# Kernel tuning notes

Hardware: AMD Instinct MI355X
Metric: run time of the kernel (lower is better)

## Reference

```python
import jax, jax.numpy as jnp
import numpy as np

N_MLPS = 256
N_BLOCKS = 8
TCODE = 13
IN_F = 3
HID = 128
OUT_F = 1
B = 256
NPTS = 2048
K = 256  # 8-bit codebook
OMEGA = 30.0

# per-layer (fan_in, fan_out) for weight reconstruction
LAYER_SHAPES = [(IN_F + TCODE, HID), (HID, HID), (HID, HID), (HID, OUT_F)]


def setup_inputs() -> dict:
    key = jax.random.key(0)
    ks = jax.random.split(key, 20)
    inp = {
        "x": jax.random.uniform(ks[0], (B, NPTS, IN_F), jnp.float32, -1.0, 1.0),
        "mlp_idx": jax.random.randint(ks[1], (B,), 0, N_MLPS, jnp.int32),
        "block_idx": jax.random.randint(ks[2], (B,), 0, N_BLOCKS, jnp.int32),
        "latent_table": jax.random.normal(ks[3], (N_MLPS, N_BLOCKS, TCODE), jnp.float32),
    }
    for l, (fi, fo) in enumerate(LAYER_SHAPES):
        bound = 1.0 / np.sqrt(fi)
        inp[f"centroids_l{l}"] = jax.random.uniform(ks[4 + 3 * l], (K,), jnp.float32, -bound, bound)
        inp[f"labels_l{l}"] = jax.random.randint(ks[5 + 3 * l], (N_MLPS * fi * fo,), 0, K, jnp.int32)
        inp[f"bias_l{l}"] = jax.random.uniform(ks[6 + 3 * l], (N_MLPS, 1, fo), jnp.float32, -bound, bound)
    return inp


def _layer(h, idx, centroids, labels, bias, fi, fo, apply_sin):
    # codebook dequant: weight.view(-1)[:] = centroids[labels]
    weight = centroids[labels].reshape(N_MLPS, fi, fo)
    # indexed bmm: torch.bmm(x, weight[indices]) + bias[indices]
    out = jnp.einsum("bni,bio->bno", h, weight[idx]) + bias[idx]
    return jnp.sin(OMEGA * out) if apply_sin else out


def reference(x, mlp_idx, block_idx, latent_table,
              centroids_l0, labels_l0, bias_l0,
              centroids_l1, labels_l1, bias_l1,
              centroids_l2, labels_l2, bias_l2,
              centroids_l3, labels_l3, bias_l3):
    # gather per-sample latent code and concat with coords
    z = latent_table[mlp_idx, block_idx]                      # [B, TCODE]
    h = jnp.concatenate(
        [x, jnp.broadcast_to(z[:, None, :], (x.shape[0], x.shape[1], TCODE))], axis=-1)
    cs = [centroids_l0, centroids_l1, centroids_l2, centroids_l3]
    ls = [labels_l0, labels_l1, labels_l2, labels_l3]
    bs = [bias_l0, bias_l1, bias_l2, bias_l3]
    for l, (fi, fo) in enumerate(LAYER_SHAPES):
        h = _layer(h, mlp_idx, cs[l], ls[l], bs[l], fi, fo, apply_sin=(l < len(LAYER_SHAPES) - 1))
    return h
```

## Files before the change

kernel.cpp:

```cpp
#include <hip/hip_runtime.h>


typedef unsigned int u32;
typedef unsigned short u16;
typedef __bf16 v8bf  __attribute__((ext_vector_type(8)));
typedef __bf16 v2bf  __attribute__((ext_vector_type(2)));
typedef float  v16f  __attribute__((ext_vector_type(16)));
typedef float  v2f   __attribute__((ext_vector_type(2)));
typedef u32    v4u   __attribute__((ext_vector_type(4)));
typedef u32    v2u   __attribute__((ext_vector_type(2)));

#define MFMA(a, b, c) __builtin_amdgcn_mfma_f32_32x32x16_bf16(a, b, c, 0, 0, 0)

#define HSTRIDE 128
#define OMEGA_S 4.774648292756860f

__device__ __forceinline__ float sinrev(float rev) {
    return __builtin_amdgcn_sinf(__builtin_amdgcn_fractf(rev));
}

__device__ __forceinline__ u32 pack2(float c) {
    __bf16 b0 = (__bf16)c;
    float  f0 = (float)b0;
    __bf16 b1 = (__bf16)(c - f0);
    return (u32)__builtin_bit_cast(u16, b0) |
           ((u32)__builtin_bit_cast(u16, b1) << 16);
}

__device__ __forceinline__ void pk2(float s0, float s1, u32& lo, u32& hi) {
    v2f s; s[0] = s0; s[1] = s1;
    v2bf l = __builtin_convertvector(s, v2bf);
    u32 lov = __builtin_bit_cast(u32, l);
    v2f lf;
    lf[0] = __builtin_bit_cast(float, lov << 16);
    lf[1] = __builtin_bit_cast(float, lov & 0xffff0000u);
    v2f r = s - lf;
    v2bf h = __builtin_convertvector(r, v2bf);
    lo = lov;
    hi = __builtin_bit_cast(u32, h);
}

__device__ __forceinline__ u32 pklo(float s0, float s1) {
    v2f s; s[0] = s0; s[1] = s1;
    v2bf l = __builtin_convertvector(s, v2bf);
    return __builtin_bit_cast(u32, l);
}

#define PLO(a, b) __builtin_amdgcn_perm((a), (b), 0x05040100u)
#define PHI(a, b) __builtin_amdgcn_perm((a), (b), 0x07060302u)

__global__ __launch_bounds__(512)
void ecnr_dequant(const float* __restrict__ cent0, const int* __restrict__ lab0,
                  const float* __restrict__ cent1, const int* __restrict__ lab1,
                  const float* __restrict__ cent2, const int* __restrict__ lab2,
                  const float* __restrict__ cent3, const int* __restrict__ lab3,
                  const float* __restrict__ bias0, const float* __restrict__ bias1,
                  const float* __restrict__ bias2,
                  u16* __restrict__ wpl1, u16* __restrict__ wpl2,
                  u16* __restrict__ w0pl, u16* __restrict__ w3pl,
                  float* __restrict__ biasc)
{
    __shared__ u32 cpk[512];
    const int t = threadIdx.x;

    if (blockIdx.x < 512) {
        const int m = blockIdx.x >> 1, L = blockIdx.x & 1;
        if (t < 256) cpk[t] = pack2((L ? cent2 : cent1)[t] * OMEGA_S);
        __syncthreads();
        const int* lab = (L ? lab2 : lab1) + (size_t)m * 16384;
        u16* base = (L ? wpl2 : wpl1) + (size_t)m * 32768;
        #pragma unroll
        for (int i = 0; i < 4; ++i) {
            const int id = i * 512 + t;
            const int n = id & 127, c = id >> 7;
            u32 g[8];
            #pragma unroll
            for (int j = 0; j < 8; ++j) g[j] = cpk[lab[(8 * c + j) * 128 + n]];
            v4u lo, hi;
            #pragma unroll
            for (int r = 0; r < 4; ++r) {
                lo[r] = PLO(g[2 * r + 1], g[2 * r]);
                hi[r] = PHI(g[2 * r + 1], g[2 * r]);
            }
            *(v4u*)(base + c * 1024 + n * 8)         = lo;
            *(v4u*)(base + 16384 + c * 1024 + n * 8) = hi;
        }
    } else {
        const int m = blockIdx.x - 512;
        if (t < 256) cpk[t] = pack2(cent0[t] * OMEGA_S);
        else         cpk[t] = pack2(cent3[t - 256]);
        __syncthreads();
        if (t < 256) {
            const int n = t & 127, c = t >> 7;
            const int* lab = lab0 + (size_t)m * 2048;
            u32 g[8];
            #pragma unroll
            for (int j = 0; j < 8; ++j) g[j] = cpk[lab[(8 * c + j) * 128 + n]];
            v4u lo, hi;
            #pragma unroll
            for (int r = 0; r < 4; ++r) {
                lo[r] = PLO(g[2 * r + 1], g[2 * r]);
                hi[r] = PHI(g[2 * r + 1], g[2 * r]);
            }
            u16* b0 = w0pl + (size_t)m * 4096;
            *(v4u*)(b0 + c * 1024 + n * 8)        = lo;
            *(v4u*)(b0 + 2048 + c * 1024 + n * 8) = hi;
        } else if (t < 384) {
            const int kk = t - 256;
            const u32 u = cpk[256 + lab3[(size_t)m * 128 + kk]];
            w3pl[(size_t)m * 256 + kk]       = (u16)u;
            w3pl[(size_t)m * 256 + 128 + kk] = (u16)(u >> 16);
        }
        if (t < 384) {
            const int li = t >> 7, kk = t & 127;
            const float* bsrc = (li == 0) ? bias0 : (li == 1) ? bias1 : bias2;
            biasc[(size_t)m * 384 + t] = bsrc[m * 128 + kk] * OMEGA_S;
        }
    }
}


#define EPI_FULL(ACC, ROWLO, ROWHI)                               \
    do {                                                          \
        _Pragma("unroll")                                         \
        for (int gg = 0; gg < 4; ++gg) {                          \
            const int wo = (((4 * nt + gg) ^ key) << 3) + 4 * q;  \
            const float s0 = sinrev((ACC)[4 * gg + 0]);           \
            const float s1 = sinrev((ACC)[4 * gg + 1]);           \
            const float s2 = sinrev((ACC)[4 * gg + 2]);           \
            const float s3 = sinrev((ACC)[4 * gg + 3]);           \
            u32 l0, h0, l1, h1;                                   \
            pk2(s0, s1, l0, h0);                                  \
            pk2(s2, s3, l1, h1);                                  \
            v2u lov, hiv;                                         \
            lov[0] = l0; lov[1] = l1;                             \
            hiv[0] = h0; hiv[1] = h1;                             \
            *(v2u*)((ROWLO) + wo) = lov;                          \
            *(v2u*)((ROWHI) + wo) = hiv;                          \
        }                                                         \
    } while (0)

#define EPI_LO(ACC, ROWLO)                                        \
    do {                                                          \
        _Pragma("unroll")                                         \
        for (int gg = 0; gg < 4; ++gg) {                          \
            const int wo = (((4 * nt + gg) ^ key) << 3) + 4 * q;  \
            const float s0 = sinrev((ACC)[4 * gg + 0]);           \
            const float s1 = sinrev((ACC)[4 * gg + 1]);           \
            const float s2 = sinrev((ACC)[4 * gg + 2]);           \
            const float s3 = sinrev((ACC)[4 * gg + 3]);           \
            v2u lov;                                              \
            lov[0] = pklo(s0, s1);                                \
            lov[1] = pklo(s2, s3);                                \
            *(v2u*)((ROWLO) + wo) = lov;                          \
        }                                                         \
    } while (0)

__global__ __launch_bounds__(256, 5)
void ecnr_fwd(const float* __restrict__ x,
              const int*   __restrict__ mlp_idx,
              const int*   __restrict__ block_idx,
              const float* __restrict__ latent,
              const float* __restrict__ bias3,
              const u16* __restrict__ wpl1, const u16* __restrict__ wpl2,
              const u16* __restrict__ w0pl, const u16* __restrict__ w3pl,
              const float* __restrict__ biasc,
              float* __restrict__ out)
{
    __shared__ __attribute__((aligned(16))) u16 Hlo[64 * HSTRIDE];
    __shared__ __attribute__((aligned(16))) u16 Hhi[64 * HSTRIDE];
    float* red = (float*)Hhi;

    const int g    = blockIdx.x;
    const int b    = ((g >> 8) << 3) | (g & 7);
    const int p0   = ((g >> 3) & 31) * 64;
    const int m    = mlp_idx[b];

    const int t  = threadIdx.x;
    const int l  = t & 63, nt = t >> 6;
    const int q  = l >> 5, ln = l & 31;
    const int nn   = nt * 32 + ln;
    const int bidx = nt * 32 + 4 * q;
    const int key  = ln & 15;

    const float* bc = biasc + (size_t)m * 384;
    const float* xpA = x + (size_t)(b * 2048 + p0 + ln) * 3;
    const float xA0 = xpA[0], xA1 = xpA[1], xA2 = xpA[2];
    const float xB0 = xpA[96], xB1 = xpA[97], xB2 = xpA[98];
    const u16* w0p = w0pl + (size_t)m * 4096 + q * 1024 + nn * 8;
    const v4u w0lo = *(const v4u*)(w0p);
    const v4u w0hi = *(const v4u*)(w0p + 2048);
    const float* zp = latent + ((size_t)m * 8 + block_idx[b]) * 13;
    float zr[8];
    #pragma unroll
    for (int j = 0; j < 8; ++j) zr[j] = zp[q * 5 + j];

    u16* rowloA = Hlo + ln * HSTRIDE;
    u16* rowhiA = Hhi + ln * HSTRIDE;
    u16* rowloB = rowloA + 32 * HSTRIDE;
    u16* rowhiB = rowhiA + 32 * HSTRIDE;

    {
        float finA[8], finB[8];
        if (q == 0) {
            finA[0] = xA0; finA[1] = xA1; finA[2] = xA2;
            finB[0] = xB0; finB[1] = xB1; finB[2] = xB2;
            #pragma unroll
            for (int j = 0; j < 5; ++j) { finA[3 + j] = zr[j]; finB[3 + j] = zr[j]; }
        } else {
            #pragma unroll
            for (int j = 0; j < 8; ++j) { finA[j] = zr[j]; finB[j] = zr[j]; }
        }
        v4u ilA, ihA, ilB, ihB;
        #pragma unroll
        for (int r = 0; r < 4; ++r) {
            u32 plo, phi;
            pk2(finA[2 * r], finA[2 * r + 1], plo, phi);
            ilA[r] = plo; ihA[r] = phi;
            pk2(finB[2 * r], finB[2 * r + 1], plo, phi);
            ilB[r] = plo; ihB[r] = phi;
        }
        const v8bf inloA = __builtin_bit_cast(v8bf, ilA);
        const v8bf inhiA = __builtin_bit_cast(v8bf, ihA);
        const v8bf inloB = __builtin_bit_cast(v8bf, ilB);
        const v8bf inhiB = __builtin_bit_cast(v8bf, ihB);
        const v8bf wl = __builtin_bit_cast(v8bf, w0lo);
        const v8bf wh = __builtin_bit_cast(v8bf, w0hi);
        v16f accA, accB;
        #pragma unroll
        for (int gg = 0; gg < 4; ++gg) {
            const float4 bv = *(const float4*)(bc + bidx + 8 * gg);
            accA[4 * gg] = bv.x; accA[4 * gg + 1] = bv.y;
            accA[4 * gg + 2] = bv.z; accA[4 * gg + 3] = bv.w;
            accB[4 * gg] = bv.x; accB[4 * gg + 1] = bv.y;
            accB[4 * gg + 2] = bv.z; accB[4 * gg + 3] = bv.w;
        }
        __builtin_amdgcn_s_setprio(1);
        accA = MFMA(wl, inloA, accA); accB = MFMA(wl, inloB, accB);
        accA = MFMA(wl, inhiA, accA); accB = MFMA(wl, inhiB, accB);
        accA = MFMA(wh, inloA, accA); accB = MFMA(wh, inloB, accB);
        __builtin_amdgcn_s_setprio(0);
        EPI_FULL(accA, rowloA, rowhiA);
        EPI_FULL(accB, rowloB, rowhiB);
    }
    __syncthreads();

    #pragma unroll 1
    for (int L = 0; L < 2; ++L) {
        const u16* Wb = (L ? wpl2 : wpl1) + (size_t)m * 32768 + q * 1024 + nn * 8;
        const float* bL = bc + 128 + (L << 7) + bidx;
        v16f accA, accB;
        #pragma unroll
        for (int gg = 0; gg < 4; ++gg) {
            const float4 bv = *(const float4*)(bL + 8 * gg);
            accA[4 * gg] = bv.x; accA[4 * gg + 1] = bv.y;
            accA[4 * gg + 2] = bv.z; accA[4 * gg + 3] = bv.w;
            accB[4 * gg] = bv.x; accB[4 * gg + 1] = bv.y;
            accB[4 * gg + 2] = bv.z; accB[4 * gg + 3] = bv.w;
        }
        #pragma unroll 1
        for (int kc = 0; kc < 8; ++kc) {
            const v4u wlv4 = *(const v4u*)(Wb + kc * 2048);
            const v4u whv4 = *(const v4u*)(Wb + kc * 2048 + 16384);
            const int ro = (((2 * kc + q) ^ key) << 3);
            const v8bf hloA = *(const v8bf*)(rowloA + ro);
            const v8bf hhiA = *(const v8bf*)(rowhiA + ro);
            const v8bf hloB = *(const v8bf*)(rowloB + ro);
            const v8bf hhiB = *(const v8bf*)(rowhiB + ro);
            const v8bf wlv = __builtin_bit_cast(v8bf, wlv4);
            const v8bf whb = __builtin_bit_cast(v8bf, whv4);
            __builtin_amdgcn_s_setprio(1);
            accA = MFMA(wlv, hloA, accA); accB = MFMA(wlv, hloB, accB);
            accA = MFMA(wlv, hhiA, accA); accB = MFMA(wlv, hhiB, accB);
            accA = MFMA(whb, hloA, accA); accB = MFMA(whb, hloB, accB);
            __builtin_amdgcn_s_setprio(0);
        }
        __syncthreads();
        if (L == 0) {
            EPI_FULL(accA, rowloA, rowhiA);
            EPI_FULL(accB, rowloB, rowhiB);
        } else {
            EPI_LO(accA, rowloA);
            EPI_LO(accB, rowloB);
        }
        __syncthreads();
    }

    {
        const u16* w3b = w3pl + (size_t)m * 256 + nt * 32 + q * 8;
        v16f aA, aB;
        #pragma unroll
        for (int r = 0; r < 16; ++r) { aA[r] = 0.0f; aB[r] = 0.0f; }
        #pragma unroll
        for (int kc = 0; kc < 2; ++kc) {
            const int o3 = (((4 * nt + 2 * kc + q) ^ key) << 3);
            const v8bf wl = *(const v8bf*)(w3b + kc * 16);
            const v8bf wh = *(const v8bf*)(w3b + 128 + kc * 16);
            const v8bf hA = *(const v8bf*)(rowloA + o3);
            const v8bf hB = *(const v8bf*)(rowloB + o3);
            __builtin_amdgcn_s_setprio(1);
            aA = MFMA(wl, hA, aA); aB = MFMA(wl, hB, aB);
            aA = MFMA(wh, hA, aA); aB = MFMA(wh, hB, aB);
            __builtin_amdgcn_s_setprio(0);
        }
        if (q == 0) {
            red[nt * 32 + ln]       = aA[0];
            red[128 + nt * 32 + ln] = aB[0];
        }
    }
    __syncthreads();

    if (t < 64) {
        const int rp = (t >> 5) * 128, rl = t & 31;
        const float o = bias3[m]
            + red[rp + rl] + red[rp + 32 + rl]
            + red[rp + 64 + rl] + red[rp + 96 + rl];
        out[(size_t)b * 2048 + p0 + t] = o;
    }
}

extern "C" void kernel_launch(void* const* d_in, const int* in_sizes, int n_in,
                              void* d_out, int out_size, void* d_ws, size_t ws_size,
                              hipStream_t stream) {
    (void)in_sizes; (void)n_in; (void)out_size; (void)ws_size;
    u16*   wpl1  = (u16*)d_ws;
    u16*   wpl2  = wpl1 + (size_t)256 * 32768;
    u16*   w0pl  = wpl2 + (size_t)256 * 32768;
    u16*   w3pl  = w0pl + (size_t)256 * 4096;
    float* biasc = (float*)(w3pl + (size_t)256 * 256);

    ecnr_dequant<<<768, 512, 0, stream>>>(
        (const float*)d_in[4],  (const int*)d_in[5],
        (const float*)d_in[7],  (const int*)d_in[8],
        (const float*)d_in[10], (const int*)d_in[11],
        (const float*)d_in[13], (const int*)d_in[14],
        (const float*)d_in[6],  (const float*)d_in[9], (const float*)d_in[12],
        wpl1, wpl2, w0pl, w3pl, biasc);

    ecnr_fwd<<<8192, 256, 0, stream>>>(
        (const float*)d_in[0], (const int*)d_in[1], (const int*)d_in[2],
        (const float*)d_in[3],
        (const float*)d_in[15],
        wpl1, wpl2, w0pl, w3pl, biasc,
        (float*)d_out);
}
```

Baseline: 229.3 us.

## Prefetch next layer's low weight planes during epilogues and unroll hidden layers

Unrolls the two hidden-layer loop iterations into separate blocks. During each previous layer's sine epilogue, it issues global loads of the next layer's eight low-plane weight vectors into registers, and it loads the final-layer weights early too, so weight-fetch latency overlaps the epilogue math and LDS writes. The inner k-loops are fully unrolled. Holding the extra weight registers forces the launch-bounds occupancy hint down from 5 to 4 blocks per CU, trading latency hiding from more waves for prefetching within each wave.

```diff
diff --git a/kernel.cpp b/kernel.cpp
--- a/kernel.cpp
+++ b/kernel.cpp
@@ -156,7 +156,7 @@
         }                                                         \
     } while (0)
 
-__global__ __launch_bounds__(256, 5)
+__global__ __launch_bounds__(256, 4)
 void ecnr_fwd(const float* __restrict__ x,
               const int*   __restrict__ mlp_idx,
               const int*   __restrict__ block_idx,
@@ -195,6 +195,10 @@
     #pragma unroll
     for (int j = 0; j < 8; ++j) zr[j] = zp[q * 5 + j];
 
+    const u16* Wb1 = wpl1 + (size_t)m * 32768 + q * 1024 + nn * 8;
+    const u16* Wb2 = wpl2 + (size_t)m * 32768 + q * 1024 + nn * 8;
+    v4u wl8[8];
+
     u16* rowloA = Hlo + ln * HSTRIDE;
     u16* rowhiA = Hhi + ln * HSTRIDE;
     u16* rowloB = rowloA + 32 * HSTRIDE;
@@ -240,15 +244,15 @@
         accA = MFMA(wl, inhiA, accA); accB = MFMA(wl, inhiB, accB);
         accA = MFMA(wh, inloA, accA); accB = MFMA(wh, inloB, accB);
         __builtin_amdgcn_s_setprio(0);
+        #pragma unroll
+        for (int kc = 0; kc < 8; ++kc) wl8[kc] = *(const v4u*)(Wb1 + kc * 2048);
         EPI_FULL(accA, rowloA, rowhiA);
         EPI_FULL(accB, rowloB, rowhiB);
     }
     __syncthreads();
 
-    #pragma unroll 1
-    for (int L = 0; L < 2; ++L) {
-        const u16* Wb = (L ? wpl2 : wpl1) + (size_t)m * 32768 + q * 1024 + nn * 8;
-        const float* bL = bc + 128 + (L << 7) + bidx;
+    {
+        const float* bL = bc + 128 + bidx;
         v16f accA, accB;
         #pragma unroll
         for (int gg = 0; gg < 4; ++gg) {
@@ -258,16 +262,15 @@
             accB[4 * gg] = bv.x; accB[4 * gg + 1] = bv.y;
             accB[4 * gg + 2] = bv.z; accB[4 * gg + 3] = bv.w;
         }
-        #pragma unroll 1
+        #pragma unroll
         for (int kc = 0; kc < 8; ++kc) {
-            const v4u wlv4 = *(const v4u*)(Wb + kc * 2048);
-            const v4u whv4 = *(const v4u*)(Wb + kc * 2048 + 16384);
+            const v4u whv4 = *(const v4u*)(Wb1 + kc * 2048 + 16384);
             const int ro = (((2 * kc + q) ^ key) << 3);
             const v8bf hloA = *(const v8bf*)(rowloA + ro);
             const v8bf hhiA = *(const v8bf*)(rowhiA + ro);
             const v8bf hloB = *(const v8bf*)(rowloB + ro);
             const v8bf hhiB = *(const v8bf*)(rowhiB + ro);
-            const v8bf wlv = __builtin_bit_cast(v8bf, wlv4);
+            const v8bf wlv = __builtin_bit_cast(v8bf, wl8[kc]);
             const v8bf whb = __builtin_bit_cast(v8bf, whv4);
             __builtin_amdgcn_s_setprio(1);
             accA = MFMA(wlv, hloA, accA); accB = MFMA(wlv, hloB, accB);
@@ -276,31 +279,67 @@
             __builtin_amdgcn_s_setprio(0);
         }
         __syncthreads();
-        if (L == 0) {
-            EPI_FULL(accA, rowloA, rowhiA);
-            EPI_FULL(accB, rowloB, rowhiB);
-        } else {
-            EPI_LO(accA, rowloA);
-            EPI_LO(accB, rowloB);
+        #pragma unroll
+        for (int kc = 0; kc < 8; ++kc) wl8[kc] = *(const v4u*)(Wb2 + kc * 2048);
+        EPI_FULL(accA, rowloA, rowhiA);
+        EPI_FULL(accB, rowloB, rowhiB);
+    }
+    __syncthreads();
+
+    v8bf w3l[2], w3h[2];
+    {
+        const float* bL = bc + 256 + bidx;
+        v16f accA, accB;
+        #pragma unroll
+        for (int gg = 0; gg < 4; ++gg) {
+            const float4 bv = *(const float4*)(bL + 8 * gg);
+            accA[4 * gg] = bv.x; accA[4 * gg + 1] = bv.y;
+            accA[4 * gg + 2] = bv.z; accA[4 * gg + 3] = bv.w;
+            accB[4 * gg] = bv.x; accB[4 * gg + 1] = bv.y;
+            accB[4 * gg + 2] = bv.z; accB[4 * gg + 3] = bv.w;
+        }
+        #pragma unroll
+        for (int kc = 0; kc < 8; ++kc) {
+            const v4u whv4 = *(const v4u*)(Wb2 + kc * 2048 + 16384);
+            const int ro = (((2 * kc + q) ^ key) << 3);
+            const v8bf hloA = *(const v8bf*)(rowloA + ro);
+            const v8bf hhiA = *(const v8bf*)(rowhiA + ro);
+            const v8bf hloB = *(const v8bf*)(rowloB + ro);
+            const v8bf hhiB = *(const v8bf*)(rowhiB + ro);
+            const v8bf wlv = __builtin_bit_cast(v8bf, wl8[kc]);
+            const v8bf whb = __builtin_bit_cast(v8bf, whv4);
+            __builtin_amdgcn_s_setprio(1);
+            accA = MFMA(wlv, hloA, accA); accB = MFMA(wlv, hloB, accB);
+            accA = MFMA(wlv, hhiA, accA); accB = MFMA(wlv, hhiB, accB);
+            accA = MFMA(whb, hloA, accA); accB = MFMA(whb, hloB, accB);
+            __builtin_amdgcn_s_setprio(0);
         }
         __syncthreads();
-    }
+        {
+            const u16* w3b = w3pl + (size_t)m * 256 + nt * 32 + q * 8;
+            #pragma unroll
+            for (int kc = 0; kc < 2; ++kc) {
+                w3l[kc] = *(const v8bf*)(w3b + kc * 16);
+                w3h[kc] = *(const v8bf*)(w3b + 128 + kc * 16);
+            }
+        }
+        EPI_LO(accA, rowloA);
+        EPI_LO(accB, rowloB);
+    }
+    __syncthreads();
 
     {
-        const u16* w3b = w3pl + (size_t)m * 256 + nt * 32 + q * 8;
         v16f aA, aB;
         #pragma unroll
         for (int r = 0; r < 16; ++r) { aA[r] = 0.0f; aB[r] = 0.0f; }
         #pragma unroll
         for (int kc = 0; kc < 2; ++kc) {
             const int o3 = (((4 * nt + 2 * kc + q) ^ key) << 3);
-            const v8bf wl = *(const v8bf*)(w3b + kc * 16);
-            const v8bf wh = *(const v8bf*)(w3b + 128 + kc * 16);
             const v8bf hA = *(const v8bf*)(rowloA + o3);
             const v8bf hB = *(const v8bf*)(rowloB + o3);
             __builtin_amdgcn_s_setprio(1);
-            aA = MFMA(wl, hA, aA); aB = MFMA(wl, hB, aB);
-            aA = MFMA(wh, hA, aA); aB = MFMA(wh, hB, aB);
+            aA = MFMA(w3l[kc], hA, aA); aB = MFMA(w3l[kc], hB, aB);
+            aA = MFMA(w3h[kc], hA, aA); aB = MFMA(w3h[kc], hB, aB);
             __builtin_amdgcn_s_setprio(0);
         }
         if (q == 0) {
```

Measured after the change: 531.9 us. 132% more time.

## Fuse final sine and output layer into register epilogue, prefetch layer weights

Applied to the files above, without the earlier changes.

The last hidden layer's sine activation and the 128-to-1 output projection now run directly on the accumulator registers with fp32 weights, reduced across lanes by a shuffle. This replaces the bf16 LDS write-back, two barriers and the output-layer MFMAs. The low-half weight vectors for each hidden layer are also loaded up front to hide global latency, and occupancy is lowered from 5 to 4 waves to make room for the extra registers. A separate shared reduction buffer is added, and the output layer now computes in full fp32 rather than the split-bf16 approximation.

```diff
diff --git a/kernel.cpp b/kernel.cpp
--- a/kernel.cpp
+++ b/kernel.cpp
@@ -40,12 +40,6 @@
     hi = __builtin_bit_cast(u32, h);
 }
 
-__device__ __forceinline__ u32 pklo(float s0, float s1) {
-    v2f s; s[0] = s0; s[1] = s1;
-    v2bf l = __builtin_convertvector(s, v2bf);
-    return __builtin_bit_cast(u32, l);
-}
-
 #define PLO(a, b) __builtin_amdgcn_perm((a), (b), 0x05040100u)
 #define PHI(a, b) __builtin_amdgcn_perm((a), (b), 0x07060302u)
 
@@ -57,7 +51,7 @@
                   const float* __restrict__ bias0, const float* __restrict__ bias1,
                   const float* __restrict__ bias2,
                   u16* __restrict__ wpl1, u16* __restrict__ wpl2,
-                  u16* __restrict__ w0pl, u16* __restrict__ w3pl,
+                  u16* __restrict__ w0pl, float* __restrict__ w3f,
                   float* __restrict__ biasc)
 {
     __shared__ u32 cpk[512];
@@ -88,7 +82,6 @@
     } else {
         const int m = blockIdx.x - 512;
         if (t < 256) cpk[t] = pack2(cent0[t] * OMEGA_S);
-        else         cpk[t] = pack2(cent3[t - 256]);
         __syncthreads();
         if (t < 256) {
             const int n = t & 127, c = t >> 7;
@@ -107,9 +100,7 @@
             *(v4u*)(b0 + 2048 + c * 1024 + n * 8) = hi;
         } else if (t < 384) {
             const int kk = t - 256;
-            const u32 u = cpk[256 + lab3[(size_t)m * 128 + kk]];
-            w3pl[(size_t)m * 256 + kk]       = (u16)u;
-            w3pl[(size_t)m * 256 + 128 + kk] = (u16)(u >> 16);
+            w3f[(size_t)m * 128 + kk] = cent3[lab3[(size_t)m * 128 + kk]];
         }
         if (t < 384) {
             const int li = t >> 7, kk = t & 127;
@@ -140,36 +131,20 @@
         }                                                         \
     } while (0)
 
-#define EPI_LO(ACC, ROWLO)                                        \
-    do {                                                          \
-        _Pragma("unroll")                                         \
-        for (int gg = 0; gg < 4; ++gg) {                          \
-            const int wo = (((4 * nt + gg) ^ key) << 3) + 4 * q;  \
-            const float s0 = sinrev((ACC)[4 * gg + 0]);           \
-            const float s1 = sinrev((ACC)[4 * gg + 1]);           \
-            const float s2 = sinrev((ACC)[4 * gg + 2]);           \
-            const float s3 = sinrev((ACC)[4 * gg + 3]);           \
-            v2u lov;                                              \
-            lov[0] = pklo(s0, s1);                                \
-            lov[1] = pklo(s2, s3);                                \
-            *(v2u*)((ROWLO) + wo) = lov;                          \
-        }                                                         \
-    } while (0)
-
-__global__ __launch_bounds__(256, 5)
+__global__ __launch_bounds__(256, 4)
 void ecnr_fwd(const float* __restrict__ x,
               const int*   __restrict__ mlp_idx,
               const int*   __restrict__ block_idx,
               const float* __restrict__ latent,
               const float* __restrict__ bias3,
               const u16* __restrict__ wpl1, const u16* __restrict__ wpl2,
-              const u16* __restrict__ w0pl, const u16* __restrict__ w3pl,
+              const u16* __restrict__ w0pl, const float* __restrict__ w3f,
               const float* __restrict__ biasc,
               float* __restrict__ out)
 {
-    __shared__ __attribute__((aligned(16))) u16 Hlo[64 * HSTRIDE];
-    __shared__ __attribute__((aligned(16))) u16 Hhi[64 * HSTRIDE];
-    float* red = (float*)Hhi;
+    __shared__ __attribute__((aligned(16))) u16   Hlo[64 * HSTRIDE];
+    __shared__ __attribute__((aligned(16))) u16   Hhi[64 * HSTRIDE];
+    __shared__ __attribute__((aligned(16))) float red[256];
 
     const int g    = blockIdx.x;
     const int b    = ((g >> 8) << 3) | (g & 7);
@@ -226,30 +201,30 @@
         const v8bf inhiB = __builtin_bit_cast(v8bf, ihB);
         const v8bf wl = __builtin_bit_cast(v8bf, w0lo);
         const v8bf wh = __builtin_bit_cast(v8bf, w0hi);
-        v16f accA, accB;
+        v16f accA0, accB0;
         #pragma unroll
         for (int gg = 0; gg < 4; ++gg) {
             const float4 bv = *(const float4*)(bc + bidx + 8 * gg);
-            accA[4 * gg] = bv.x; accA[4 * gg + 1] = bv.y;
-            accA[4 * gg + 2] = bv.z; accA[4 * gg + 3] = bv.w;
-            accB[4 * gg] = bv.x; accB[4 * gg + 1] = bv.y;
-            accB[4 * gg + 2] = bv.z; accB[4 * gg + 3] = bv.w;
+            accA0[4 * gg] = bv.x; accA0[4 * gg + 1] = bv.y;
+            accA0[4 * gg + 2] = bv.z; accA0[4 * gg + 3] = bv.w;
+            accB0[4 * gg] = bv.x; accB0[4 * gg + 1] = bv.y;
+            accB0[4 * gg + 2] = bv.z; accB0[4 * gg + 3] = bv.w;
         }
         __builtin_amdgcn_s_setprio(1);
-        accA = MFMA(wl, inloA, accA); accB = MFMA(wl, inloB, accB);
-        accA = MFMA(wl, inhiA, accA); accB = MFMA(wl, inhiB, accB);
-        accA = MFMA(wh, inloA, accA); accB = MFMA(wh, inloB, accB);
+        accA0 = MFMA(wl, inloA, accA0); accB0 = MFMA(wl, inloB, accB0);
+        accA0 = MFMA(wl, inhiA, accA0); accB0 = MFMA(wl, inhiB, accB0);
+        accA0 = MFMA(wh, inloA, accA0); accB0 = MFMA(wh, inloB, accB0);
         __builtin_amdgcn_s_setprio(0);
-        EPI_FULL(accA, rowloA, rowhiA);
-        EPI_FULL(accB, rowloB, rowhiB);
+        EPI_FULL(accA0, rowloA, rowhiA);
+        EPI_FULL(accB0, rowloB, rowhiB);
     }
     __syncthreads();
 
+    v16f accA, accB;
     #pragma unroll 1
     for (int L = 0; L < 2; ++L) {
         const u16* Wb = (L ? wpl2 : wpl1) + (size_t)m * 32768 + q * 1024 + nn * 8;
         const float* bL = bc + 128 + (L << 7) + bidx;
-        v16f accA, accB;
         #pragma unroll
         for (int gg = 0; gg < 4; ++gg) {
             const float4 bv = *(const float4*)(bL + 8 * gg);
@@ -258,16 +233,19 @@
             accB[4 * gg] = bv.x; accB[4 * gg + 1] = bv.y;
             accB[4 * gg + 2] = bv.z; accB[4 * gg + 3] = bv.w;
         }
-        #pragma unroll 1
+        v4u wl8[8];
+        #pragma unroll
+        for (int kc = 0; kc < 8; ++kc)
+            wl8[kc] = *(const v4u*)(Wb + kc * 2048);
+        #pragma unroll
         for (int kc = 0; kc < 8; ++kc) {
-            const v4u wlv4 = *(const v4u*)(Wb + kc * 2048);
             const v4u whv4 = *(const v4u*)(Wb + kc * 2048 + 16384);
             const int ro = (((2 * kc + q) ^ key) << 3);
             const v8bf hloA = *(const v8bf*)(rowloA + ro);
             const v8bf hhiA = *(const v8bf*)(rowhiA + ro);
             const v8bf hloB = *(const v8bf*)(rowloB + ro);
             const v8bf hhiB = *(const v8bf*)(rowhiB + ro);
-            const v8bf wlv = __builtin_bit_cast(v8bf, wlv4);
+            const v8bf wlv = __builtin_bit_cast(v8bf, wl8[kc]);
             const v8bf whb = __builtin_bit_cast(v8bf, whv4);
             __builtin_amdgcn_s_setprio(1);
             accA = MFMA(wlv, hloA, accA); accB = MFMA(wlv, hloB, accB);
@@ -275,37 +253,42 @@
             accA = MFMA(whb, hloA, accA); accB = MFMA(whb, hloB, accB);
             __builtin_amdgcn_s_setprio(0);
         }
-        __syncthreads();
         if (L == 0) {
+            __syncthreads();
             EPI_FULL(accA, rowloA, rowhiA);
             EPI_FULL(accB, rowloB, rowhiB);
-        } else {
-            EPI_LO(accA, rowloA);
-            EPI_LO(accB, rowloB);
-        }
-        __syncthreads();
+            __syncthreads();
+        }
     }
 
     {
-        const u16* w3b = w3pl + (size_t)m * 256 + nt * 32 + q * 8;
-        v16f aA, aB;
-        #pragma unroll
-        for (int r = 0; r < 16; ++r) { aA[r] = 0.0f; aB[r] = 0.0f; }
-        #pragma unroll
-        for (int kc = 0; kc < 2; ++kc) {
-            const int o3 = (((4 * nt + 2 * kc + q) ^ key) << 3);
-            const v8bf wl = *(const v8bf*)(w3b + kc * 16);
-            const v8bf wh = *(const v8bf*)(w3b + 128 + kc * 16);
-            const v8bf hA = *(const v8bf*)(rowloA + o3);
-            const v8bf hB = *(const v8bf*)(rowloB + o3);
-            __builtin_amdgcn_s_setprio(1);
-            aA = MFMA(wl, hA, aA); aB = MFMA(wl, hB, aB);
-            aA = MFMA(wh, hA, aA); aB = MFMA(wh, hB, aB);
-            __builtin_amdgcn_s_setprio(0);
-        }
+        const float* w3p = w3f + (size_t)m * 128 + nt * 32 + 4 * q;
+        const float4 wv0 = *(const float4*)(w3p);
+        const float4 wv1 = *(const float4*)(w3p + 8);
+        const float4 wv2 = *(const float4*)(w3p + 16);
+        const float4 wv3 = *(const float4*)(w3p + 24);
+        float pA, pB;
+        pA  = wv0.x * sinrev(accA[0]);  pB  = wv0.x * sinrev(accB[0]);
+        pA += wv0.y * sinrev(accA[1]);  pB += wv0.y * sinrev(accB[1]);
+        pA += wv0.z * sinrev(accA[2]);  pB += wv0.z * sinrev(accB[2]);
+        pA += wv0.w * sinrev(accA[3]);  pB += wv0.w * sinrev(accB[3]);
+        pA += wv1.x * sinrev(accA[4]);  pB += wv1.x * sinrev(accB[4]);
+        pA += wv1.y * sinrev(accA[5]);  pB += wv1.y * sinrev(accB[5]);
+        pA += wv1.z * sinrev(accA[6]);  pB += wv1.z * sinrev(accB[6]);
+        pA += wv1.w * sinrev(accA[7]);  pB += wv1.w * sinrev(accB[7]);
+        pA += wv2.x * sinrev(accA[8]);  pB += wv2.x * sinrev(accB[8]);
+        pA += wv2.y * sinrev(accA[9]);  pB += wv2.y * sinrev(accB[9]);
+        pA += wv2.z * sinrev(accA[10]); pB += wv2.z * sinrev(accB[10]);
+        pA += wv2.w * sinrev(accA[11]); pB += wv2.w * sinrev(accB[11]);
+        pA += wv3.x * sinrev(accA[12]); pB += wv3.x * sinrev(accB[12]);
+        pA += wv3.y * sinrev(accA[13]); pB += wv3.y * sinrev(accB[13]);
+        pA += wv3.z * sinrev(accA[14]); pB += wv3.z * sinrev(accB[14]);
+        pA += wv3.w * sinrev(accA[15]); pB += wv3.w * sinrev(accB[15]);
+        pA += __shfl_xor(pA, 32);
+        pB += __shfl_xor(pB, 32);
         if (q == 0) {
-            red[nt * 32 + ln]       = aA[0];
-            red[128 + nt * 32 + ln] = aB[0];
+            red[nt * 32 + ln]       = pA;
+            red[128 + nt * 32 + ln] = pB;
         }
     }
     __syncthreads();
@@ -326,8 +309,8 @@
     u16*   wpl1  = (u16*)d_ws;
     u16*   wpl2  = wpl1 + (size_t)256 * 32768;
     u16*   w0pl  = wpl2 + (size_t)256 * 32768;
-    u16*   w3pl  = w0pl + (size_t)256 * 4096;
-    float* biasc = (float*)(w3pl + (size_t)256 * 256);
+    float* w3f   = (float*)(w0pl + (size_t)256 * 4096);
+    float* biasc = w3f + (size_t)256 * 128;
 
     ecnr_dequant<<<768, 512, 0, stream>>>(
         (const float*)d_in[4],  (const int*)d_in[5],
@@ -335,12 +318,12 @@
         (const float*)d_in[10], (const int*)d_in[11],
         (const float*)d_in[13], (const int*)d_in[14],
         (const float*)d_in[6],  (const float*)d_in[9], (const float*)d_in[12],
-        wpl1, wpl2, w0pl, w3pl, biasc);
+        wpl1, wpl2, w0pl, w3f, biasc);
 
     ecnr_fwd<<<8192, 256, 0, stream>>>(
         (const float*)d_in[0], (const int*)d_in[1], (const int*)d_in[2],
         (const float*)d_in[3],
         (const float*)d_in[15],
-        wpl1, wpl2, w0pl, w3pl, biasc,
+        wpl1, wpl2, w0pl, w3f, biasc,
         (float*)d_out);
 }
```

Result: faster. 224.4 us (-2.1%).
